# Performance work log

Measured on AMD Instinct MI355X. Metric: run time of the kernel, lower is better.

The kernel has to match this reference:

```python
import jax, jax.numpy as jnp
import numpy as np

B, S, D, H, DFF, HID = 512, 100, 512, 2, 256, 230
DH = D // H


def _ln_torch(x, g, b, eps=1e-5):
    # nn.LayerNorm: biased variance, eps inside sqrt
    m = x.mean(-1, keepdims=True)
    v = ((x - m) ** 2).mean(-1, keepdims=True)
    return g * (x - m) / jnp.sqrt(v + eps) + b


def _ln_custom(x, g, b, eps=1e-6):
    # repo's custom LayerNorm: unbiased std (torch.std default), eps added to std
    m = x.mean(-1, keepdims=True)
    s = jnp.std(x, axis=-1, ddof=1, keepdims=True)
    return g * (x - m) / (s + eps) + b


def setup_inputs() -> dict:
    key = jax.random.key(0)
    ks = jax.random.split(key, 32)
    w = lambda k, shape: jax.random.normal(k, shape, jnp.float32) * 0.02
    return {
        'inp': jax.random.normal(ks[0], (B, S, D), jnp.float32),
        'mask': jax.random.randint(ks[1], (B, S), 0, 2).astype(jnp.int32),
        'gate': jax.random.uniform(ks[2], (B, S, S), jnp.float32),
        'wv': w(ks[3], (D, D)), 'bv': jnp.zeros((D,), jnp.float32),
        'fc_w': w(ks[4], (D, D)), 'fc_b': jnp.zeros((D,), jnp.float32),
        'lnm_g': jnp.ones((D,), jnp.float32), 'lnm_b': jnp.zeros((D,), jnp.float32),
        'w1': w(ks[5], (DFF, D)), 'b1': jnp.zeros((DFF,), jnp.float32),
        'w2': w(ks[6], (D, DFF)), 'b2': jnp.zeros((D,), jnp.float32),
        'lpc_w': w(ks[7], (D, D)), 'lpc_b': jnp.zeros((D,), jnp.float32),
        'lnc_g': jnp.ones((D,), jnp.float32), 'lnc_b': jnp.zeros((D,), jnp.float32),
        'pwf_w': w(ks[8], (DFF, D)), 'pwf_b': jnp.zeros((DFF,), jnp.float32),
        'lpi_w': w(ks[9], (D, DFF)), 'lpi_b': jnp.zeros((D,), jnp.float32),
        'lni_g': jnp.ones((D,), jnp.float32), 'lni_b': jnp.zeros((D,), jnp.float32),
        'lnf_g': jnp.ones((D,), jnp.float32), 'lnf_b': jnp.zeros((D,), jnp.float32),
        'mlpf_w': w(ks[10], (HID, D)), 'mlpf_b': jnp.zeros((HID,), jnp.float32),
    }


def reference(inp, mask, gate, wv, bv, fc_w, fc_b, lnm_g, lnm_b, w1, b1, w2, b2,
              lpc_w, lpc_b, lnc_g, lnc_b, pwf_w, pwf_b, lpi_w, lpi_b,
              lni_g, lni_b, lnf_g, lnf_b, mlpf_w, mlpf_b):
    b = inp.shape[0]
    maskf = mask.astype(jnp.float32)
    masks = maskf[:, :, None] * maskf[:, None, :]              # [B,S,S]
    # In the source, attention scores are FULLY replaced by the mask via
    # torch.where(mask==0, 1e-8, mask); the q/k projections and the gate
    # multiplication have no effect on the output (dead computation).
    attn = jnp.where(masks == 0, jnp.float32(1e-8), masks)
    p = jax.nn.softmax(attn, axis=-1)                          # [B,S,S] (same for both heads)
    v = (inp @ wv.T + bv).reshape(b, S, H, DH)                 # [B,S,H,dh]
    ctx = jnp.einsum('bst,bthd->bshd', p, v).reshape(b, S, D)  # head-concat order matches torch
    mha = _ln_torch(ctx @ fc_w.T + fc_b + inp, lnm_g, lnm_b)   # dropout = identity (eval)
    # 1x1-conv FFN + custom LN
    ffn = jax.nn.relu(mha @ w1.T + b1) @ w2.T + b2
    ctx2 = _ln_custom(ffn + mha, lni_g, lni_b)
    # context projection applied to BOTH original inp and ffn output (shared weights)
    res_inp = _ln_custom((inp @ lpc_w.T + lpc_b) + (ctx2 @ lpc_w.T + lpc_b), lnc_g, lnc_b)
    rv = jax.nn.relu(res_inp @ pwf_w.T + pwf_b) @ lpi_w.T + lpi_b
    res = _ln_custom(rv + res_inp, lnf_g, lnf_b)
    return res @ mlpf_w.T + mlpf_b                             # x_for_att: [B,S,230]
```

## Files before the change

### kernel.cpp

```cpp
#include <hip/hip_runtime.h>

#define BB  512
#define SS  100
#define DD  512
#define DFF 256
#define HIDN 230
#define LDA 520

typedef unsigned short u16;
typedef unsigned int   u32;
typedef __attribute__((ext_vector_type(8))) short v8s;
typedef __attribute__((ext_vector_type(4))) float v4f;

__device__ __forceinline__ float b2f(u16 u){
  union { u32 i; float f; } v; v.i = ((u32)u) << 16; return v.f;
}
__device__ __forceinline__ u16 f2b(float f){
  union { float f; u32 i; } v; v.f = f;
  u32 r = (v.i + 0x7fffu + ((v.i >> 16) & 1u)) >> 16;
  return (u16)r;
}
__device__ __forceinline__ float rsum16(float s){
  #pragma unroll
  for (int o = 1; o < 16; o <<= 1) s += __shfl_xor(s, o, 64);
  return s;
}

template<int K, int NT>
__device__ __forceinline__ void mm_pk(const u16* __restrict__ arow,
                                      const u16* __restrict__ b0, v4f* acc){
  constexpr int NC = K / 32;
  v8s b[NT];
  #pragma unroll
  for (int i = 0; i < NT; i++)
    b[i] = *(const v8s*)(b0 + (size_t)i*64*K);
  v8s a = *(const v8s*)(arow);
  #pragma unroll
  for (int kc = 0; kc < NC; kc++){
    v8s bn[NT];
    if (kc + 1 < NC){
      #pragma unroll
      for (int i = 0; i < NT; i++)
        bn[i] = *(const v8s*)(b0 + (size_t)i*64*K + (kc+1)*512);
    }
    v8s an = (kc + 1 < NC) ? *(const v8s*)(arow + (kc+1)*32) : a;
    #pragma unroll
    for (int i = 0; i < NT; i++)
      acc[i] = __builtin_amdgcn_mfma_f32_16x16x32_bf16(a, b[i], acc[i], 0, 0, 0);
    #pragma unroll
    for (int i = 0; i < NT; i++) b[i] = bn[i];
    a = an;
  }
}

template<bool ADDX>
__device__ __forceinline__ void ln_custom_pass(int lrow, int lc,
    const u16 (*src)[LDA], u16 (*dst)[LDA], const u32* xp,
    const u16* __restrict__ g, const u16* __restrict__ bb)
{
  float v[32]; float s = 0.f;
  #pragma unroll
  for (int j = 0; j < 32; j++){ int col = lc + j*16; float x = b2f(src[lrow][col]); v[j] = x; s += x; }
  s = rsum16(s);
  float mean = s * (1.0f/512.0f);
  float vs = 0.f;
  #pragma unroll
  for (int j = 0; j < 32; j++){ float d = v[j] - mean; vs += d*d; }
  vs = rsum16(vs);
  float inv = 1.0f / (sqrtf(vs * (1.0f/511.0f)) + 1e-6f);
  #pragma unroll
  for (int j = 0; j < 32; j++){
    int col = lc + j*16;
    float r = b2f(g[col]) * (v[j] - mean) * inv + b2f(bb[col]);
    if (ADDX){
      u32 p = xp[j >> 1];
      u16 xu = (j & 1) ? (u16)(p >> 16) : (u16)(p & 0xffffu);
      r += b2f(xu);
    }
    dst[lrow][col] = f2b(r);
  }
}

#define NSEG 20
struct CvtArgs {
  const float* src[NSEG];
  u16* dst;
  int off[NSEG];
  int n[NSEG];
  int ncs[6];
  int nin[6];
};
__global__ __launch_bounds__(256) void k_cvt(CvtArgs a){
  int total = a.off[NSEG-1] + a.n[NSEG-1];
  for (int i = blockIdx.x*blockDim.x + threadIdx.x; i < total; i += gridDim.x*blockDim.x){
    int s = 0;
    #pragma unroll
    for (int j = 1; j < NSEG; j++) if (i >= a.off[j]) s = j;
    int o = i - a.off[s];
    if (s < 6){
      int j  = o & 7;
      int l  = (o >> 3) & 63;
      int m  = l & 15, q = l >> 4;
      int rest = o >> 9;
      int ncs = a.ncs[s];
      int kc = rest & ((1 << ncs) - 1);
      int t  = rest >> ncs;
      int col = t*16 + m;
      int k   = kc*32 + q*8 + j;
      int K   = 32 << ncs;
      float v = (col < a.nin[s]) ? a.src[s][(size_t)col*K + k] : 0.f;
      a.dst[i] = f2b(v);
    } else {
      a.dst[i] = f2b(a.src[s][o]);
    }
  }
}

__global__ __launch_bounds__(512) void k_batch(
    const float* __restrict__ inp, const int* __restrict__ mask,
    const float* __restrict__ wv, const float* __restrict__ bv,
    const float* __restrict__ fcw, const float* __restrict__ fcb,
    float* __restrict__ a_m, float* __restrict__ a_u)
{
  __shared__ float sia[DD], sim[DD], cm[DD], cu[DD];
  __shared__ int smask[SS];
  const int b = blockIdx.x, t = threadIdx.x;
  const int lane = t & 63, w8 = t >> 6;
  if (t < SS) smask[t] = mask[b*SS + t];
  __syncthreads();
  const float* base = inp + (size_t)b * SS * DD;
  float aa = 0.f, am = 0.f; int n = 0;
  for (int s = 0; s < SS; s++){
    float x = base[s*DD + t];
    int mk = smask[s];
    aa += x; n += (mk != 0); if (mk) am += x;
  }
  sia[t] = aa; sim[t] = am;
  __syncthreads();
  const float e0 = expf(1e-8f - 1.0f);
  const float denom = (float)n + (float)(SS - n) * e0;
  const float p1 = 1.0f / denom, p0 = e0 / denom;
  {
    float s_a[8], s_m[8];
    #pragma unroll
    for (int j = 0; j < 8; j++){ s_a[j] = sia[lane*8 + j]; s_m[j] = sim[lane*8 + j]; }
    for (int rr = 0; rr < 64; rr++){
      int d = w8*64 + rr;
      const float4* wr = (const float4*)(wv + (size_t)d * DD + lane*8);
      float4 wA = wr[0], wB = wr[1];
      float sva = wA.x*s_a[0] + wA.y*s_a[1] + wA.z*s_a[2] + wA.w*s_a[3]
                + wB.x*s_a[4] + wB.y*s_a[5] + wB.z*s_a[6] + wB.w*s_a[7];
      float svm = wA.x*s_m[0] + wA.y*s_m[1] + wA.z*s_m[2] + wA.w*s_m[3]
                + wB.x*s_m[4] + wB.y*s_m[5] + wB.z*s_m[6] + wB.w*s_m[7];
      #pragma unroll
      for (int o = 1; o < 64; o <<= 1){ sva += __shfl_xor(sva, o, 64); svm += __shfl_xor(svm, o, 64); }
      if (lane == 0){
        float bvd = bv[d];
        sva += (float)SS * bvd;
        svm += (float)n  * bvd;
        cm[d] = p1*svm + p0*(sva - svm);
        cu[d] = sva * (1.0f/(float)SS);
      }
    }
  }
  __syncthreads();
  {
    float c_m[8], c_u[8];
    #pragma unroll
    for (int j = 0; j < 8; j++){ c_m[j] = cm[lane*8 + j]; c_u[j] = cu[lane*8 + j]; }
    for (int rr = 0; rr < 64; rr++){
      int d = w8*64 + rr;
      const float4* fr = (const float4*)(fcw + (size_t)d * DD + lane*8);
      float4 wA = fr[0], wB = fr[1];
      float xm = wA.x*c_m[0] + wA.y*c_m[1] + wA.z*c_m[2] + wA.w*c_m[3]
               + wB.x*c_m[4] + wB.y*c_m[5] + wB.z*c_m[6] + wB.w*c_m[7];
      float xu = wA.x*c_u[0] + wA.y*c_u[1] + wA.z*c_u[2] + wA.w*c_u[3]
               + wB.x*c_u[4] + wB.y*c_u[5] + wB.z*c_u[6] + wB.w*c_u[7];
      #pragma unroll
      for (int o = 1; o < 64; o <<= 1){ xm += __shfl_xor(xm, o, 64); xu += __shfl_xor(xu, o, 64); }
      if (lane == 0){
        float fb = fcb[d];
        a_m[(size_t)b*DD + d] = xm + fb;
        a_u[(size_t)b*DD + d] = xu + fb;
      }
    }
  }
}

__global__ __launch_bounds__(256, 4) void k_main(
    const float* __restrict__ inp, const int* __restrict__ mask,
    const u16* __restrict__ lnm_g, const u16* __restrict__ lnm_b,
    const u16* __restrict__ w1,   const u16* __restrict__ b1,
    const u16* __restrict__ w2,   const u16* __restrict__ b2,
    const u16* __restrict__ lpc_w, const u16* __restrict__ lpc_b,
    const u16* __restrict__ lnc_g, const u16* __restrict__ lnc_b,
    const u16* __restrict__ pwf_w, const u16* __restrict__ pwf_b,
    const u16* __restrict__ lpi_w, const u16* __restrict__ lpi_b,
    const u16* __restrict__ lni_g, const u16* __restrict__ lni_b,
    const u16* __restrict__ lnf_g, const u16* __restrict__ lnf_b,
    const u16* __restrict__ mlpf_w, const u16* __restrict__ mlpf_b,
    const float* __restrict__ a_m, const float* __restrict__ a_u,
    float* __restrict__ out)
{
  __shared__ __align__(16) u16 A[16][LDA];
  __shared__ __align__(16) u16 O[16][LDA];
  __shared__ int marr[16];

  const int tid  = threadIdx.x;
  const int lane = tid & 63, wid = tid >> 6;
  const int m = lane & 15, q = lane >> 4;
  const int r0 = blockIdx.x * 16;
  const int lrow = tid >> 4, lc = tid & 15;

  {
    float4 va[4], vb[4];
    #pragma unroll
    for (int c = 0; c < 4; c++){
      int e = c*2048 + tid*8;
      int row = e >> 9, col = e & 511;
      const float4* p = (const float4*)(inp + (size_t)(r0 + row) * DD + col);
      va[c] = p[0]; vb[c] = p[1];
    }
    if (tid < 16) marr[tid] = mask[r0 + tid];
    #pragma unroll
    for (int c = 0; c < 4; c++){
      int e = c*2048 + tid*8;
      int row = e >> 9, col = e & 511;
      uint4 o;
      o.x = (u32)f2b(va[c].x) | ((u32)f2b(va[c].y) << 16);
      o.y = (u32)f2b(va[c].z) | ((u32)f2b(va[c].w) << 16);
      o.z = (u32)f2b(vb[c].x) | ((u32)f2b(vb[c].y) << 16);
      o.w = (u32)f2b(vb[c].z) | ((u32)f2b(vb[c].w) << 16);
      *(uint4*)&O[row][col] = o;
    }
  }
  __syncthreads();

  u32 xp[16];
  {
    int Rg = r0 + lrow;
    int bi = Rg / SS;
    const float* asel = (marr[lrow] ? a_m : a_u) + (size_t)bi * DD;
    float v[32]; float s = 0.f;
    #pragma unroll
    for (int j = 0; j < 32; j++){
      int col = lc + j*16;
      u16 xu = O[lrow][col];
      if ((j & 1) == 0) xp[j >> 1] = (u32)xu;
      else              xp[j >> 1] |= ((u32)xu << 16);
      float x = asel[col] + b2f(xu);
      v[j] = x; s += x;
    }
    s = rsum16(s);
    float mean = s * (1.0f/512.0f);
    float vs = 0.f;
    #pragma unroll
    for (int j = 0; j < 32; j++){ float d = v[j] - mean; vs += d*d; }
    vs = rsum16(vs);
    float inv = 1.0f / sqrtf(vs * (1.0f/512.0f) + 1e-5f);
    #pragma unroll
    for (int j = 0; j < 32; j++){
      int col = lc + j*16;
      float r = b2f(lnm_g[col]) * (v[j] - mean) * inv + b2f(lnm_b[col]);
      A[lrow][col] = f2b(r);
    }
  }
  __syncthreads();

  {
    v4f acc[4];
    #pragma unroll
    for (int i = 0; i < 4; i++) acc[i] = (v4f){0.f,0.f,0.f,0.f};
    mm_pk<512,4>(&A[m][q*8], w1 + (size_t)wid*16*512 + lane*8, acc);
    #pragma unroll
    for (int ti = 0; ti < 4; ti++){
      int col = (wid + ti*4)*16 + m;
      float bias = b2f(b1[col]);
      #pragma unroll
      for (int i = 0; i < 4; i++){
        float val = acc[ti][i] + bias;
        O[q*4+i][col] = f2b(val > 0.f ? val : 0.f);
      }
    }
  }
  __syncthreads();

  {
    v4f acc[8];
    #pragma unroll
    for (int i = 0; i < 8; i++) acc[i] = (v4f){0.f,0.f,0.f,0.f};
    const u16* a0 = &O[m][q*8];
    mm_pk<256,4>(a0, w2 + (size_t)(wid     )*16*256 + lane*8, acc);
    mm_pk<256,4>(a0, w2 + (size_t)(wid + 16)*16*256 + lane*8, acc + 4);
    __syncthreads();
    #pragma unroll
    for (int ti = 0; ti < 8; ti++){
      int t = (ti < 4) ? (wid + ti*4) : (wid + 16 + (ti-4)*4);
      int col = t*16 + m;
      float bias = b2f(b2[col]);
      #pragma unroll
      for (int i = 0; i < 4; i++){
        int row = q*4 + i;
        O[row][col] = f2b(acc[ti][i] + bias + b2f(A[row][col]));
      }
    }
  }
  __syncthreads();

  ln_custom_pass<true>(lrow, lc, O, A, xp, lni_g, lni_b);
  __syncthreads();

  {
    v4f acc[8];
    #pragma unroll
    for (int i = 0; i < 8; i++) acc[i] = (v4f){0.f,0.f,0.f,0.f};
    mm_pk<512,8>(&A[m][q*8], lpc_w + (size_t)wid*16*512 + lane*8, acc);
    #pragma unroll
    for (int ti = 0; ti < 8; ti++){
      int col = (wid + ti*4)*16 + m;
      float bias = 2.0f * b2f(lpc_b[col]);
      #pragma unroll
      for (int i = 0; i < 4; i++) O[q*4+i][col] = f2b(acc[ti][i] + bias);
    }
  }
  __syncthreads();

  ln_custom_pass<false>(lrow, lc, O, A, nullptr, lnc_g, lnc_b);
  __syncthreads();

  {
    v4f acc[4];
    #pragma unroll
    for (int i = 0; i < 4; i++) acc[i] = (v4f){0.f,0.f,0.f,0.f};
    mm_pk<512,4>(&A[m][q*8], pwf_w + (size_t)wid*16*512 + lane*8, acc);
    #pragma unroll
    for (int ti = 0; ti < 4; ti++){
      int col = (wid + ti*4)*16 + m;
      float bias = b2f(pwf_b[col]);
      #pragma unroll
      for (int i = 0; i < 4; i++){
        float val = acc[ti][i] + bias;
        O[q*4+i][col] = f2b(val > 0.f ? val : 0.f);
      }
    }
  }
  __syncthreads();

  {
    v4f acc[8];
    #pragma unroll
    for (int i = 0; i < 8; i++) acc[i] = (v4f){0.f,0.f,0.f,0.f};
    mm_pk<256,8>(&O[m][q*8], lpi_w + (size_t)wid*16*256 + lane*8, acc);
    __syncthreads();
    #pragma unroll
    for (int ti = 0; ti < 8; ti++){
      int col = (wid + ti*4)*16 + m;
      float bias = b2f(lpi_b[col]);
      #pragma unroll
      for (int i = 0; i < 4; i++){
        int row = q*4 + i;
        O[row][col] = f2b(acc[ti][i] + bias + b2f(A[row][col]));
      }
    }
  }
  __syncthreads();

  ln_custom_pass<false>(lrow, lc, O, A, nullptr, lnf_g, lnf_b);
  __syncthreads();

  {
    v4f acc[4];
    #pragma unroll
    for (int i = 0; i < 4; i++) acc[i] = (v4f){0.f,0.f,0.f,0.f};
    mm_pk<512,4>(&A[m][q*8], mlpf_w + (size_t)wid*16*512 + lane*8, acc);
    #pragma unroll
    for (int ti = 0; ti < 4; ti++){
      int t = wid + ti*4;
      int col = t*16 + m;
      if (col < HIDN){
        float bias = b2f(mlpf_b[col]);
        #pragma unroll
        for (int i = 0; i < 4; i++){
          int row = q*4 + i;
          out[(size_t)(r0 + row)*HIDN + col] = acc[ti][i] + bias;
        }
      }
    }
  }
}

extern "C" void kernel_launch(void* const* d_in, const int* in_sizes, int n_in,
                              void* d_out, int out_size, void* d_ws, size_t ws_size,
                              hipStream_t stream)
{
  const float* inp    = (const float*)d_in[0];
  const int*   mask   = (const int*)d_in[1];
  const float* wv     = (const float*)d_in[3];
  const float* bv     = (const float*)d_in[4];
  const float* fc_w   = (const float*)d_in[5];
  const float* fc_b   = (const float*)d_in[6];

  float* a_m = (float*)d_ws;
  float* a_u = a_m + (size_t)BB * DD;
  u16* bfb = (u16*)((char*)d_ws + 2u * BB * DD * sizeof(float));

  const int OW1   = 0;
  const int OW2   = OW1   + DFF*DD;
  const int OLPC  = OW2   + DD*DFF;
  const int OPWF  = OLPC  + DD*DD;
  const int OLPI  = OPWF  + DFF*DD;
  const int OMLPF = OLPI  + DD*DFF;
  int voff = OMLPF + 256*DD;
  const int OLNMG = voff; voff += DD;
  const int OLNMB = voff; voff += DD;
  const int OB1   = voff; voff += DFF;
  const int OB2   = voff; voff += DD;
  const int OLPCB = voff; voff += DD;
  const int OLNCG = voff; voff += DD;
  const int OLNCB = voff; voff += DD;
  const int OPWFB = voff; voff += DFF;
  const int OLPIB = voff; voff += DD;
  const int OLNIG = voff; voff += DD;
  const int OLNIB = voff; voff += DD;
  const int OLNFG = voff; voff += DD;
  const int OLNFB = voff; voff += DD;
  const int OMLPFB = voff; voff += HIDN;

  CvtArgs ca;
  const int srcidx[NSEG] = {9, 11, 13, 17, 19, 25,
                            7, 8, 10, 12, 14, 15, 16, 18, 20, 21, 22, 23, 24, 26};
  const int offs[NSEG]   = {OW1, OW2, OLPC, OPWF, OLPI, OMLPF,
                            OLNMG, OLNMB, OB1, OB2, OLPCB, OLNCG, OLNCB, OPWFB,
                            OLPIB, OLNIG, OLNIB, OLNFG, OLNFB, OMLPFB};
  const int lens[NSEG]   = {DFF*DD, DD*DFF, DD*DD, DFF*DD, DD*DFF, 256*DD,
                            DD, DD, DFF, DD, DD, DD, DD, DFF, DD, DD, DD, DD, DD, HIDN};
  const int ncss[6] = {4, 3, 4, 4, 3, 4};
  const int nins[6] = {DFF, DD, DD, DFF, DD, HIDN};
  for (int i = 0; i < NSEG; i++){
    ca.src[i] = (const float*)d_in[srcidx[i]];
    ca.off[i] = offs[i];
    ca.n[i]   = lens[i];
  }
  for (int i = 0; i < 6; i++){ ca.ncs[i] = ncss[i]; ca.nin[i] = nins[i]; }
  ca.dst = bfb;

  k_cvt<<<512, 256, 0, stream>>>(ca);
  k_batch<<<BB, 512, 0, stream>>>(inp, mask, wv, bv, fc_w, fc_b, a_m, a_u);
  k_main<<<(BB*SS)/16, 256, 0, stream>>>(inp, mask,
      bfb + OLNMG, bfb + OLNMB,
      bfb + OW1,   bfb + OB1,
      bfb + OW2,   bfb + OB2,
      bfb + OLPC,  bfb + OLPCB,
      bfb + OLNCG, bfb + OLNCB,
      bfb + OPWF,  bfb + OPWFB,
      bfb + OLPI,  bfb + OLPIB,
      bfb + OLNIG, bfb + OLNIB,
      bfb + OLNFG, bfb + OLNFB,
      bfb + OMLPF, bfb + OMLPFB,
      a_m, a_u, (float*)d_out);
}
```

Baseline: 585.3 us.

## Process 32 rows per block with 8 waves reusing each weight fragment twice

```diff
diff --git a/kernel.cpp b/kernel.cpp
--- a/kernel.cpp
+++ b/kernel.cpp
@@ -26,30 +26,39 @@
   return s;
 }
 
-template<int K, int NT>
-__device__ __forceinline__ void mm_pk(const u16* __restrict__ arow,
-                                      const u16* __restrict__ b0, v4f* acc){
+template<int K, int NJ>
+__device__ __forceinline__ void mm_2m(const u16* __restrict__ a0r,
+                                      const u16* __restrict__ a1r,
+                                      const u16* __restrict__ b0,
+                                      v4f (*acc)[NJ]){
   constexpr int NC = K / 32;
-  v8s b[NT];
-  #pragma unroll
-  for (int i = 0; i < NT; i++)
-    b[i] = *(const v8s*)(b0 + (size_t)i*64*K);
-  v8s a = *(const v8s*)(arow);
+  v8s b[NJ];
+  #pragma unroll
+  for (int j = 0; j < NJ; j++) b[j] = *(const v8s*)(b0 + (size_t)j*128*K);
+  v8s a0 = *(const v8s*)(a0r);
+  v8s a1 = *(const v8s*)(a1r);
   #pragma unroll
   for (int kc = 0; kc < NC; kc++){
-    v8s bn[NT];
+    v8s bn[NJ]; v8s a0n, a1n;
     if (kc + 1 < NC){
       #pragma unroll
-      for (int i = 0; i < NT; i++)
-        bn[i] = *(const v8s*)(b0 + (size_t)i*64*K + (kc+1)*512);
-    }
-    v8s an = (kc + 1 < NC) ? *(const v8s*)(arow + (kc+1)*32) : a;
-    #pragma unroll
-    for (int i = 0; i < NT; i++)
-      acc[i] = __builtin_amdgcn_mfma_f32_16x16x32_bf16(a, b[i], acc[i], 0, 0, 0);
-    #pragma unroll
-    for (int i = 0; i < NT; i++) b[i] = bn[i];
-    a = an;
+      for (int j = 0; j < NJ; j++)
+        bn[j] = *(const v8s*)(b0 + (size_t)j*128*K + (kc+1)*512);
+      a0n = *(const v8s*)(a0r + (kc+1)*32);
+      a1n = *(const v8s*)(a1r + (kc+1)*32);
+    } else {
+      #pragma unroll
+      for (int j = 0; j < NJ; j++) bn[j] = b[j];
+      a0n = a0; a1n = a1;
+    }
+    #pragma unroll
+    for (int j = 0; j < NJ; j++){
+      acc[0][j] = __builtin_amdgcn_mfma_f32_16x16x32_bf16(a0, b[j], acc[0][j], 0, 0, 0);
+      acc[1][j] = __builtin_amdgcn_mfma_f32_16x16x32_bf16(a1, b[j], acc[1][j], 0, 0, 0);
+    }
+    #pragma unroll
+    for (int j = 0; j < NJ; j++) b[j] = bn[j];
+    a0 = a0n; a1 = a1n;
   }
 }
 
@@ -187,7 +196,7 @@
   }
 }
 
-__global__ __launch_bounds__(256, 4) void k_main(
+__global__ __launch_bounds__(512, 4) void k_main(
     const float* __restrict__ inp, const int* __restrict__ mask,
     const u16* __restrict__ lnm_g, const u16* __restrict__ lnm_b,
     const u16* __restrict__ w1,   const u16* __restrict__ b1,
@@ -202,29 +211,29 @@
     const float* __restrict__ a_m, const float* __restrict__ a_u,
     float* __restrict__ out)
 {
-  __shared__ __align__(16) u16 A[16][LDA];
-  __shared__ __align__(16) u16 O[16][LDA];
-  __shared__ int marr[16];
+  __shared__ __align__(16) u16 A[32][LDA];
+  __shared__ __align__(16) u16 O[32][LDA];
+  __shared__ int marr[32];
 
   const int tid  = threadIdx.x;
   const int lane = tid & 63, wid = tid >> 6;
   const int m = lane & 15, q = lane >> 4;
-  const int r0 = blockIdx.x * 16;
+  const int r0 = blockIdx.x * 32;
   const int lrow = tid >> 4, lc = tid & 15;
 
   {
+    if (tid < 32) marr[tid] = mask[r0 + tid];
     float4 va[4], vb[4];
     #pragma unroll
     for (int c = 0; c < 4; c++){
-      int e = c*2048 + tid*8;
+      int e = c*4096 + tid*8;
       int row = e >> 9, col = e & 511;
       const float4* p = (const float4*)(inp + (size_t)(r0 + row) * DD + col);
       va[c] = p[0]; vb[c] = p[1];
     }
-    if (tid < 16) marr[tid] = mask[r0 + tid];
     #pragma unroll
     for (int c = 0; c < 4; c++){
-      int e = c*2048 + tid*8;
+      int e = c*4096 + tid*8;
       int row = e >> 9, col = e & 511;
       uint4 o;
       o.x = (u32)f2b(va[c].x) | ((u32)f2b(va[c].y) << 16);
@@ -268,41 +277,46 @@
   __syncthreads();
 
   {
-    v4f acc[4];
-    #pragma unroll
-    for (int i = 0; i < 4; i++) acc[i] = (v4f){0.f,0.f,0.f,0.f};
-    mm_pk<512,4>(&A[m][q*8], w1 + (size_t)wid*16*512 + lane*8, acc);
-    #pragma unroll
-    for (int ti = 0; ti < 4; ti++){
-      int col = (wid + ti*4)*16 + m;
+    v4f acc[2][2];
+    #pragma unroll
+    for (int mt = 0; mt < 2; mt++)
+      #pragma unroll
+      for (int j = 0; j < 2; j++) acc[mt][j] = (v4f){0.f,0.f,0.f,0.f};
+    mm_2m<512,2>(&A[m][q*8], &A[m+16][q*8], w1 + (size_t)wid*16*512 + lane*8, acc);
+    #pragma unroll
+    for (int j = 0; j < 2; j++){
+      int col = (wid + 8*j)*16 + m;
       float bias = b2f(b1[col]);
       #pragma unroll
-      for (int i = 0; i < 4; i++){
-        float val = acc[ti][i] + bias;
-        O[q*4+i][col] = f2b(val > 0.f ? val : 0.f);
-      }
-    }
-  }
-  __syncthreads();
-
-  {
-    v4f acc[8];
-    #pragma unroll
-    for (int i = 0; i < 8; i++) acc[i] = (v4f){0.f,0.f,0.f,0.f};
-    const u16* a0 = &O[m][q*8];
-    mm_pk<256,4>(a0, w2 + (size_t)(wid     )*16*256 + lane*8, acc);
-    mm_pk<256,4>(a0, w2 + (size_t)(wid + 16)*16*256 + lane*8, acc + 4);
+      for (int mt = 0; mt < 2; mt++)
+        #pragma unroll
+        for (int i = 0; i < 4; i++){
+          float val = acc[mt][j][i] + bias;
+          O[mt*16 + q*4 + i][col] = f2b(val > 0.f ? val : 0.f);
+        }
+    }
+  }
+  __syncthreads();
+
+  {
+    v4f acc[2][4];
+    #pragma unroll
+    for (int mt = 0; mt < 2; mt++)
+      #pragma unroll
+      for (int j = 0; j < 4; j++) acc[mt][j] = (v4f){0.f,0.f,0.f,0.f};
+    mm_2m<256,4>(&O[m][q*8], &O[m+16][q*8], w2 + (size_t)wid*16*256 + lane*8, acc);
     __syncthreads();
     #pragma unroll
-    for (int ti = 0; ti < 8; ti++){
-      int t = (ti < 4) ? (wid + ti*4) : (wid + 16 + (ti-4)*4);
-      int col = t*16 + m;
+    for (int j = 0; j < 4; j++){
+      int col = (wid + 8*j)*16 + m;
       float bias = b2f(b2[col]);
       #pragma unroll
-      for (int i = 0; i < 4; i++){
-        int row = q*4 + i;
-        O[row][col] = f2b(acc[ti][i] + bias + b2f(A[row][col]));
-      }
+      for (int mt = 0; mt < 2; mt++)
+        #pragma unroll
+        for (int i = 0; i < 4; i++){
+          int row = mt*16 + q*4 + i;
+          O[row][col] = f2b(acc[mt][j][i] + bias + b2f(A[row][col]));
+        }
     }
   }
   __syncthreads();
@@ -311,16 +325,20 @@
   __syncthreads();
 
   {
-    v4f acc[8];
-    #pragma unroll
-    for (int i = 0; i < 8; i++) acc[i] = (v4f){0.f,0.f,0.f,0.f};
-    mm_pk<512,8>(&A[m][q*8], lpc_w + (size_t)wid*16*512 + lane*8, acc);
-    #pragma unroll
-    for (int ti = 0; ti < 8; ti++){
-      int col = (wid + ti*4)*16 + m;
+    v4f acc[2][4];
+    #pragma unroll
+    for (int mt = 0; mt < 2; mt++)
+      #pragma unroll
+      for (int j = 0; j < 4; j++) acc[mt][j] = (v4f){0.f,0.f,0.f,0.f};
+    mm_2m<512,4>(&A[m][q*8], &A[m+16][q*8], lpc_w + (size_t)wid*16*512 + lane*8, acc);
+    #pragma unroll
+    for (int j = 0; j < 4; j++){
+      int col = (wid + 8*j)*16 + m;
       float bias = 2.0f * b2f(lpc_b[col]);
       #pragma unroll
-      for (int i = 0; i < 4; i++) O[q*4+i][col] = f2b(acc[ti][i] + bias);
+      for (int mt = 0; mt < 2; mt++)
+        #pragma unroll
+        for (int i = 0; i < 4; i++) O[mt*16 + q*4 + i][col] = f2b(acc[mt][j][i] + bias);
     }
   }
   __syncthreads();
@@ -329,38 +347,46 @@
   __syncthreads();
 
   {
-    v4f acc[4];
-    #pragma unroll
-    for (int i = 0; i < 4; i++) acc[i] = (v4f){0.f,0.f,0.f,0.f};
-    mm_pk<512,4>(&A[m][q*8], pwf_w + (size_t)wid*16*512 + lane*8, acc);
-    #pragma unroll
-    for (int ti = 0; ti < 4; ti++){
-      int col = (wid + ti*4)*16 + m;
+    v4f acc[2][2];
+    #pragma unroll
+    for (int mt = 0; mt < 2; mt++)
+      #pragma unroll
+      for (int j = 0; j < 2; j++) acc[mt][j] = (v4f){0.f,0.f,0.f,0.f};
+    mm_2m<512,2>(&A[m][q*8], &A[m+16][q*8], pwf_w + (size_t)wid*16*512 + lane*8, acc);
+    #pragma unroll
+    for (int j = 0; j < 2; j++){
+      int col = (wid + 8*j)*16 + m;
       float bias = b2f(pwf_b[col]);
       #pragma unroll
-      for (int i = 0; i < 4; i++){
-        float val = acc[ti][i] + bias;
-        O[q*4+i][col] = f2b(val > 0.f ? val : 0.f);
-      }
-    }
-  }
-  __syncthreads();
-
-  {
-    v4f acc[8];
-    #pragma unroll
-    for (int i = 0; i < 8; i++) acc[i] = (v4f){0.f,0.f,0.f,0.f};
-    mm_pk<256,8>(&O[m][q*8], lpi_w + (size_t)wid*16*256 + lane*8, acc);
+      for (int mt = 0; mt < 2; mt++)
+        #pragma unroll
+        for (int i = 0; i < 4; i++){
+          float val = acc[mt][j][i] + bias;
+          O[mt*16 + q*4 + i][col] = f2b(val > 0.f ? val : 0.f);
+        }
+    }
+  }
+  __syncthreads();
+
+  {
+    v4f acc[2][4];
+    #pragma unroll
+    for (int mt = 0; mt < 2; mt++)
+      #pragma unroll
+      for (int j = 0; j < 4; j++) acc[mt][j] = (v4f){0.f,0.f,0.f,0.f};
+    mm_2m<256,4>(&O[m][q*8], &O[m+16][q*8], lpi_w + (size_t)wid*16*256 + lane*8, acc);
     __syncthreads();
     #pragma unroll
-    for (int ti = 0; ti < 8; ti++){
-      int col = (wid + ti*4)*16 + m;
+    for (int j = 0; j < 4; j++){
+      int col = (wid + 8*j)*16 + m;
       float bias = b2f(lpi_b[col]);
       #pragma unroll
-      for (int i = 0; i < 4; i++){
-        int row = q*4 + i;
-        O[row][col] = f2b(acc[ti][i] + bias + b2f(A[row][col]));
-      }
+      for (int mt = 0; mt < 2; mt++)
+        #pragma unroll
+        for (int i = 0; i < 4; i++){
+          int row = mt*16 + q*4 + i;
+          O[row][col] = f2b(acc[mt][j][i] + bias + b2f(A[row][col]));
+        }
     }
   }
   __syncthreads();
@@ -369,21 +395,24 @@
   __syncthreads();
 
   {
-    v4f acc[4];
-    #pragma unroll
-    for (int i = 0; i < 4; i++) acc[i] = (v4f){0.f,0.f,0.f,0.f};
-    mm_pk<512,4>(&A[m][q*8], mlpf_w + (size_t)wid*16*512 + lane*8, acc);
-    #pragma unroll
-    for (int ti = 0; ti < 4; ti++){
-      int t = wid + ti*4;
-      int col = t*16 + m;
+    v4f acc[2][2];
+    #pragma unroll
+    for (int mt = 0; mt < 2; mt++)
+      #pragma unroll
+      for (int j = 0; j < 2; j++) acc[mt][j] = (v4f){0.f,0.f,0.f,0.f};
+    mm_2m<512,2>(&A[m][q*8], &A[m+16][q*8], mlpf_w + (size_t)wid*16*512 + lane*8, acc);
+    #pragma unroll
+    for (int j = 0; j < 2; j++){
+      int col = (wid + 8*j)*16 + m;
       if (col < HIDN){
         float bias = b2f(mlpf_b[col]);
         #pragma unroll
-        for (int i = 0; i < 4; i++){
-          int row = q*4 + i;
-          out[(size_t)(r0 + row)*HIDN + col] = acc[ti][i] + bias;
-        }
+        for (int mt = 0; mt < 2; mt++)
+          #pragma unroll
+          for (int i = 0; i < 4; i++){
+            int row = mt*16 + q*4 + i;
+            out[(size_t)(r0 + row)*HIDN + col] = acc[mt][j][i] + bias;
+          }
       }
     }
   }
@@ -446,7 +475,7 @@
 
   k_cvt<<<512, 256, 0, stream>>>(ca);
   k_batch<<<BB, 512, 0, stream>>>(inp, mask, wv, bv, fc_w, fc_b, a_m, a_u);
-  k_main<<<(BB*SS)/16, 256, 0, stream>>>(inp, mask,
+  k_main<<<(BB*SS)/32, 512, 0, stream>>>(inp, mask,
       bfb + OLNMG, bfb + OLNMB,
       bfb + OW1,   bfb + OB1,
       bfb + OW2,   bfb + OB2,
```

After: 588.0 us. No clear change (+0.5%).

## Stage weight tiles in LDS via async global-to-LDS loads and fuse prep kernels

Applied to the files above, without the earlier changes.

```diff
diff --git a/kernel.cpp b/kernel.cpp
--- a/kernel.cpp
+++ b/kernel.cpp
@@ -26,30 +26,44 @@
   return s;
 }
 
-template<int K, int NT>
-__device__ __forceinline__ void mm_pk(const u16* __restrict__ arow,
-                                      const u16* __restrict__ b0, v4f* acc){
+__device__ __forceinline__ void gl16(const u16* g, u16* l){
+  __builtin_amdgcn_global_load_lds(
+      (const __attribute__((address_space(1))) void*)g,
+      (__attribute__((address_space(3))) void*)l, 16, 0, 0);
+}
+
+template<int K, int NH>
+__device__ __forceinline__ void gemm_lds(const u16 (*Asrc)[LDA], const u16* __restrict__ W,
+                                         u16 (*Bb)[8192], int s0, int lane, int m, int q,
+                                         v4f* acc){
   constexpr int NC = K / 32;
-  v8s b[NT];
+  {
+    const u16* src = W + (size_t)s0*16*K + lane*8;
+    u16* dst = Bb[0] + s0*512;
+    #pragma unroll
+    for (int i = 0; i < 4; i++) gl16(src + (size_t)i*16*K, dst + i*512);
+  }
+  __syncthreads();
   #pragma unroll
-  for (int i = 0; i < NT; i++)
-    b[i] = *(const v8s*)(b0 + (size_t)i*64*K);
-  v8s a = *(const v8s*)(arow);
-  #pragma unroll
-  for (int kc = 0; kc < NC; kc++){
-    v8s bn[NT];
-    if (kc + 1 < NC){
-      #pragma unroll
-      for (int i = 0; i < NT; i++)
-        bn[i] = *(const v8s*)(b0 + (size_t)i*64*K + (kc+1)*512);
-    }
-    v8s an = (kc + 1 < NC) ? *(const v8s*)(arow + (kc+1)*32) : a;
-    #pragma unroll
-    for (int i = 0; i < NT; i++)
-      acc[i] = __builtin_amdgcn_mfma_f32_16x16x32_bf16(a, b[i], acc[i], 0, 0, 0);
-    #pragma unroll
-    for (int i = 0; i < NT; i++) b[i] = bn[i];
-    a = an;
+  for (int nh = 0; nh < NH; nh++){
+    for (int kc = 0; kc < NC; kc++){
+      int nkc = kc + 1, nnh = nh;
+      if (nkc == NC){ nkc = 0; nnh++; }
+      if (nnh < NH){
+        const u16* src = W + (size_t)(nnh*16 + s0)*16*K + nkc*512 + lane*8;
+        u16* dst = Bb[(kc + 1) & 1] + s0*512;
+        #pragma unroll
+        for (int i = 0; i < 4; i++) gl16(src + (size_t)i*16*K, dst + i*512);
+      }
+      v8s a = *(const v8s*)(&Asrc[m][kc*32 + q*8]);
+      const u16* bp = Bb[kc & 1] + s0*512 + lane*8;
+      #pragma unroll
+      for (int i = 0; i < 4; i++){
+        v8s b = *(const v8s*)(bp + i*512);
+        acc[nh*4 + i] = __builtin_amdgcn_mfma_f32_16x16x32_bf16(a, b, acc[nh*4 + i], 0, 0, 0);
+      }
+      __syncthreads();
+    }
   }
 }
 
@@ -90,38 +104,37 @@
   int ncs[6];
   int nin[6];
 };
-__global__ __launch_bounds__(256) void k_cvt(CvtArgs a){
-  int total = a.off[NSEG-1] + a.n[NSEG-1];
-  for (int i = blockIdx.x*blockDim.x + threadIdx.x; i < total; i += gridDim.x*blockDim.x){
-    int s = 0;
-    #pragma unroll
-    for (int j = 1; j < NSEG; j++) if (i >= a.off[j]) s = j;
-    int o = i - a.off[s];
-    if (s < 6){
-      int j  = o & 7;
-      int l  = (o >> 3) & 63;
-      int m  = l & 15, q = l >> 4;
-      int rest = o >> 9;
-      int ncs = a.ncs[s];
-      int kc = rest & ((1 << ncs) - 1);
-      int t  = rest >> ncs;
-      int col = t*16 + m;
-      int k   = kc*32 + q*8 + j;
-      int K   = 32 << ncs;
-      float v = (col < a.nin[s]) ? a.src[s][(size_t)col*K + k] : 0.f;
-      a.dst[i] = f2b(v);
-    } else {
-      a.dst[i] = f2b(a.src[s][o]);
-    }
-  }
-}
-
-__global__ __launch_bounds__(512) void k_batch(
+__global__ __launch_bounds__(512) void k_pre(CvtArgs a,
     const float* __restrict__ inp, const int* __restrict__ mask,
     const float* __restrict__ wv, const float* __restrict__ bv,
     const float* __restrict__ fcw, const float* __restrict__ fcb,
     float* __restrict__ a_m, float* __restrict__ a_u)
 {
+  {
+    int total = a.off[NSEG-1] + a.n[NSEG-1];
+    for (int i = blockIdx.x*blockDim.x + threadIdx.x; i < total; i += gridDim.x*blockDim.x){
+      int s = 0;
+      #pragma unroll
+      for (int j = 1; j < NSEG; j++) if (i >= a.off[j]) s = j;
+      int o = i - a.off[s];
+      if (s < 6){
+        int j  = o & 7;
+        int l  = (o >> 3) & 63;
+        int m  = l & 15, q = l >> 4;
+        int rest = o >> 9;
+        int ncs = a.ncs[s];
+        int kc = rest & ((1 << ncs) - 1);
+        int t  = rest >> ncs;
+        int col = t*16 + m;
+        int k   = kc*32 + q*8 + j;
+        int K   = 32 << ncs;
+        float v = (col < a.nin[s]) ? a.src[s][(size_t)col*K + k] : 0.f;
+        a.dst[i] = f2b(v);
+      } else {
+        a.dst[i] = f2b(a.src[s][o]);
+      }
+    }
+  }
   __shared__ float sia[DD], sim[DD], cm[DD], cu[DD];
   __shared__ int smask[SS];
   const int b = blockIdx.x, t = threadIdx.x;
@@ -187,7 +200,7 @@
   }
 }
 
-__global__ __launch_bounds__(256, 4) void k_main(
+__global__ __launch_bounds__(256, 2) void k_main(
     const float* __restrict__ inp, const int* __restrict__ mask,
     const u16* __restrict__ lnm_g, const u16* __restrict__ lnm_b,
     const u16* __restrict__ w1,   const u16* __restrict__ b1,
@@ -204,15 +217,18 @@
 {
   __shared__ __align__(16) u16 A[16][LDA];
   __shared__ __align__(16) u16 O[16][LDA];
+  __shared__ __align__(16) u16 Bb[2][8192];
   __shared__ int marr[16];
 
   const int tid  = threadIdx.x;
   const int lane = tid & 63, wid = tid >> 6;
   const int m = lane & 15, q = lane >> 4;
+  const int s0 = wid * 4;
   const int r0 = blockIdx.x * 16;
   const int lrow = tid >> 4, lc = tid & 15;
 
   {
+    if (tid < 16) marr[tid] = mask[r0 + tid];
     float4 va[4], vb[4];
     #pragma unroll
     for (int c = 0; c < 4; c++){
@@ -221,7 +237,6 @@
       const float4* p = (const float4*)(inp + (size_t)(r0 + row) * DD + col);
       va[c] = p[0]; vb[c] = p[1];
     }
-    if (tid < 16) marr[tid] = mask[r0 + tid];
     #pragma unroll
     for (int c = 0; c < 4; c++){
       int e = c*2048 + tid*8;
@@ -271,118 +286,118 @@
     v4f acc[4];
     #pragma unroll
     for (int i = 0; i < 4; i++) acc[i] = (v4f){0.f,0.f,0.f,0.f};
-    mm_pk<512,4>(&A[m][q*8], w1 + (size_t)wid*16*512 + lane*8, acc);
-    #pragma unroll
-    for (int ti = 0; ti < 4; ti++){
-      int col = (wid + ti*4)*16 + m;
+    gemm_lds<512,1>(A, w1, Bb, s0, lane, m, q, acc);
+    #pragma unroll
+    for (int i = 0; i < 4; i++){
+      int col = (s0 + i)*16 + m;
       float bias = b2f(b1[col]);
       #pragma unroll
+      for (int r = 0; r < 4; r++){
+        float val = acc[i][r] + bias;
+        O[q*4+r][col] = f2b(val > 0.f ? val : 0.f);
+      }
+    }
+  }
+  __syncthreads();
+
+  {
+    v4f acc[8];
+    #pragma unroll
+    for (int i = 0; i < 8; i++) acc[i] = (v4f){0.f,0.f,0.f,0.f};
+    gemm_lds<256,2>(O, w2, Bb, s0, lane, m, q, acc);
+    #pragma unroll
+    for (int nh = 0; nh < 2; nh++)
+      #pragma unroll
       for (int i = 0; i < 4; i++){
-        float val = acc[ti][i] + bias;
-        O[q*4+i][col] = f2b(val > 0.f ? val : 0.f);
-      }
-    }
-  }
+        int col = nh*256 + (s0 + i)*16 + m;
+        float bias = b2f(b2[col]);
+        #pragma unroll
+        for (int r = 0; r < 4; r++){
+          int row = q*4 + r;
+          O[row][col] = f2b(acc[nh*4+i][r] + bias + b2f(A[row][col]));
+        }
+      }
+  }
+  __syncthreads();
+
+  ln_custom_pass<true>(lrow, lc, O, A, xp, lni_g, lni_b);
   __syncthreads();
 
   {
     v4f acc[8];
     #pragma unroll
     for (int i = 0; i < 8; i++) acc[i] = (v4f){0.f,0.f,0.f,0.f};
-    const u16* a0 = &O[m][q*8];
-    mm_pk<256,4>(a0, w2 + (size_t)(wid     )*16*256 + lane*8, acc);
-    mm_pk<256,4>(a0, w2 + (size_t)(wid + 16)*16*256 + lane*8, acc + 4);
-    __syncthreads();
-    #pragma unroll
-    for (int ti = 0; ti < 8; ti++){
-      int t = (ti < 4) ? (wid + ti*4) : (wid + 16 + (ti-4)*4);
-      int col = t*16 + m;
-      float bias = b2f(b2[col]);
+    gemm_lds<512,2>(A, lpc_w, Bb, s0, lane, m, q, acc);
+    #pragma unroll
+    for (int nh = 0; nh < 2; nh++)
       #pragma unroll
       for (int i = 0; i < 4; i++){
-        int row = q*4 + i;
-        O[row][col] = f2b(acc[ti][i] + bias + b2f(A[row][col]));
-      }
-    }
-  }
-  __syncthreads();
-
-  ln_custom_pass<true>(lrow, lc, O, A, xp, lni_g, lni_b);
+        int col = nh*256 + (s0 + i)*16 + m;
+        float bias = 2.0f * b2f(lpc_b[col]);
+        #pragma unroll
+        for (int r = 0; r < 4; r++) O[q*4+r][col] = f2b(acc[nh*4+i][r] + bias);
+      }
+  }
+  __syncthreads();
+
+  ln_custom_pass<false>(lrow, lc, O, A, nullptr, lnc_g, lnc_b);
+  __syncthreads();
+
+  {
+    v4f acc[4];
+    #pragma unroll
+    for (int i = 0; i < 4; i++) acc[i] = (v4f){0.f,0.f,0.f,0.f};
+    gemm_lds<512,1>(A, pwf_w, Bb, s0, lane, m, q, acc);
+    #pragma unroll
+    for (int i = 0; i < 4; i++){
+      int col = (s0 + i)*16 + m;
+      float bias = b2f(pwf_b[col]);
+      #pragma unroll
+      for (int r = 0; r < 4; r++){
+        float val = acc[i][r] + bias;
+        O[q*4+r][col] = f2b(val > 0.f ? val : 0.f);
+      }
+    }
+  }
   __syncthreads();
 
   {
     v4f acc[8];
     #pragma unroll
     for (int i = 0; i < 8; i++) acc[i] = (v4f){0.f,0.f,0.f,0.f};
-    mm_pk<512,8>(&A[m][q*8], lpc_w + (size_t)wid*16*512 + lane*8, acc);
-    #pragma unroll
-    for (int ti = 0; ti < 8; ti++){
-      int col = (wid + ti*4)*16 + m;
-      float bias = 2.0f * b2f(lpc_b[col]);
-      #pragma unroll
-      for (int i = 0; i < 4; i++) O[q*4+i][col] = f2b(acc[ti][i] + bias);
-    }
-  }
-  __syncthreads();
-
-  ln_custom_pass<false>(lrow, lc, O, A, nullptr, lnc_g, lnc_b);
+    gemm_lds<256,2>(O, lpi_w, Bb, s0, lane, m, q, acc);
+    #pragma unroll
+    for (int nh = 0; nh < 2; nh++)
+      #pragma unroll
+      for (int i = 0; i < 4; i++){
+        int col = nh*256 + (s0 + i)*16 + m;
+        float bias = b2f(lpi_b[col]);
+        #pragma unroll
+        for (int r = 0; r < 4; r++){
+          int row = q*4 + r;
+          O[row][col] = f2b(acc[nh*4+i][r] + bias + b2f(A[row][col]));
+        }
+      }
+  }
+  __syncthreads();
+
+  ln_custom_pass<false>(lrow, lc, O, A, nullptr, lnf_g, lnf_b);
   __syncthreads();
 
   {
     v4f acc[4];
     #pragma unroll
     for (int i = 0; i < 4; i++) acc[i] = (v4f){0.f,0.f,0.f,0.f};
-    mm_pk<512,4>(&A[m][q*8], pwf_w + (size_t)wid*16*512 + lane*8, acc);
-    #pragma unroll
-    for (int ti = 0; ti < 4; ti++){
-      int col = (wid + ti*4)*16 + m;
-      float bias = b2f(pwf_b[col]);
-      #pragma unroll
-      for (int i = 0; i < 4; i++){
-        float val = acc[ti][i] + bias;
-        O[q*4+i][col] = f2b(val > 0.f ? val : 0.f);
-      }
-    }
-  }
-  __syncthreads();
-
-  {
-    v4f acc[8];
-    #pragma unroll
-    for (int i = 0; i < 8; i++) acc[i] = (v4f){0.f,0.f,0.f,0.f};
-    mm_pk<256,8>(&O[m][q*8], lpi_w + (size_t)wid*16*256 + lane*8, acc);
-    __syncthreads();
-    #pragma unroll
-    for (int ti = 0; ti < 8; ti++){
-      int col = (wid + ti*4)*16 + m;
-      float bias = b2f(lpi_b[col]);
-      #pragma unroll
-      for (int i = 0; i < 4; i++){
-        int row = q*4 + i;
-        O[row][col] = f2b(acc[ti][i] + bias + b2f(A[row][col]));
-      }
-    }
-  }
-  __syncthreads();
-
-  ln_custom_pass<false>(lrow, lc, O, A, nullptr, lnf_g, lnf_b);
-  __syncthreads();
-
-  {
-    v4f acc[4];
-    #pragma unroll
-    for (int i = 0; i < 4; i++) acc[i] = (v4f){0.f,0.f,0.f,0.f};
-    mm_pk<512,4>(&A[m][q*8], mlpf_w + (size_t)wid*16*512 + lane*8, acc);
-    #pragma unroll
-    for (int ti = 0; ti < 4; ti++){
-      int t = wid + ti*4;
-      int col = t*16 + m;
+    gemm_lds<512,1>(A, mlpf_w, Bb, s0, lane, m, q, acc);
+    #pragma unroll
+    for (int i = 0; i < 4; i++){
+      int col = (s0 + i)*16 + m;
       if (col < HIDN){
         float bias = b2f(mlpf_b[col]);
         #pragma unroll
-        for (int i = 0; i < 4; i++){
-          int row = q*4 + i;
-          out[(size_t)(r0 + row)*HIDN + col] = acc[ti][i] + bias;
+        for (int r = 0; r < 4; r++){
+          int row = q*4 + r;
+          out[(size_t)(r0 + row)*HIDN + col] = acc[i][r] + bias;
         }
       }
     }
@@ -444,8 +459,7 @@
   for (int i = 0; i < 6; i++){ ca.ncs[i] = ncss[i]; ca.nin[i] = nins[i]; }
   ca.dst = bfb;
 
-  k_cvt<<<512, 256, 0, stream>>>(ca);
-  k_batch<<<BB, 512, 0, stream>>>(inp, mask, wv, bv, fc_w, fc_b, a_m, a_u);
+  k_pre<<<BB, 512, 0, stream>>>(ca, inp, mask, wv, bv, fc_w, fc_b, a_m, a_u);
   k_main<<<(BB*SS)/16, 256, 0, stream>>>(inp, mask,
       bfb + OLNMG, bfb + OLNMB,
       bfb + OW1,   bfb + OB1,
```

Result: slower. 978.8 us (+67.2%).
